# Optimization experiments

Measured on AMD Instinct MI355X. Metric: run time of the kernel, lower is better.

Reference implementation:

```python
import jax, jax.numpy as jnp
import numpy as np

T, B, V, F = 30, 32, 32, 128   # len_pred, batch, n_vehicles, feature_size
L, LF = 256, 64                # n_lanes, lane_feature_size
H = 8                          # n_heads
DH = F // H                    # head dim
HIST = 10                      # leading mask dim reduced by any()


def setup_inputs() -> dict:
    key = jax.random.key(0)
    ks = jax.random.split(key, 16)
    s = 0.05
    return {
        "vehicles":    jax.random.normal(ks[0], (T, B, V, F), jnp.float32),
        "initial_pos": jax.random.normal(ks[1], (T, B, V, F), jnp.float32),
        "lanes":       jax.random.normal(ks[2], (B, L, LF), jnp.float32),
        "mask_lanes":  jax.random.randint(ks[3], (HIST, B, L), 0, 2).astype(bool),
        # key_lanes / value_lanes: Linear(LF -> F)
        "Wk": jax.random.normal(ks[4], (F, LF), jnp.float32) * s,
        "bk": jax.random.normal(ks[5], (F,), jnp.float32) * s,
        "Wv": jax.random.normal(ks[6], (F, LF), jnp.float32) * s,
        "bv": jax.random.normal(ks[7], (F,), jnp.float32) * s,
        # query / relation_lanes: Conv2d(F, F, (1,1)) == pointwise Linear(F -> F)
        "Wq": jax.random.normal(ks[8], (F, F), jnp.float32) * s,
        "bq": jax.random.normal(ks[9], (F,), jnp.float32) * s,
        "Wr": jax.random.normal(ks[10], (F, F), jnp.float32) * s,
        "br": jax.random.normal(ks[11], (F,), jnp.float32) * s,
        # attention_combine: Linear(F -> F)
        "Wc": jax.random.normal(ks[12], (F, F), jnp.float32) * s,
        "bc": jax.random.normal(ks[13], (F,), jnp.float32) * s,
    }


def reference(vehicles, initial_pos, lanes, mask_lanes,
              Wk, bk, Wv, bv, Wq, bq, Wr, br, Wc, bc):
    v = vehicles + initial_pos                                   # [T,B,V,F]
    # lane projections -> [B,H,L,DH]
    k = (lanes @ Wk.T + bk).reshape(B, L, H, DH).transpose(0, 2, 1, 3)
    val = (lanes @ Wv.T + bv).reshape(B, L, H, DH).transpose(0, 2, 1, 3)
    # vehicle projections (1x1 conv == linear over feature dim) -> [T,B,H,V,DH]
    q = (v @ Wq.T + bq).reshape(T, B, V, H, DH).transpose(0, 1, 3, 2, 4)
    r = (v @ Wr.T + br).reshape(T, B, V, H, DH).transpose(0, 1, 3, 2, 4)
    # mask: any over leading dims -> [B,L]
    mask = jnp.any(mask_lanes, axis=0)
    scores = jnp.einsum('tbhvd,bhld->tbhvl', q, k) / jnp.sqrt(jnp.float32(DH))
    scores = jnp.where(mask[None, :, None, None, :], scores, jnp.float32(-1e9))
    p = jax.nn.softmax(scores, axis=-1)                          # [T,B,H,V,L]
    att = jnp.exp(jnp.einsum('tbhvl,bhld->tbhvd', p, jax.nn.log_sigmoid(val)))
    # faithful to original: raw reshape [T,B,H,V,DH] -> [T,B,V,F] (no permute back)
    out = (r * att).reshape(T, B, V, F)
    return out @ Wc.T + bc + v - 2.0 * initial_pos
```

## Files before the change

kernel.cpp:

```cpp
#include <hip/hip_runtime.h>
#include <hip/hip_bf16.h>
#include <math.h>

#define T_ 30
#define B_ 32
#define V_ 32
#define F_ 128
#define L_ 256
#define LF_ 64
#define H_ 8
#define DH_ 16
#define HIST_ 10

typedef __attribute__((ext_vector_type(4))) float floatx4;
typedef __attribute__((ext_vector_type(8))) short shortx8;
typedef __attribute__((ext_vector_type(4))) unsigned short ushortx4;

#define MFMA_BF16(a, b, c) __builtin_amdgcn_mfma_f32_16x16x32_bf16(a, b, c, 0, 0, 0)

__device__ inline unsigned short f2bf_rne(float x) {
    unsigned int u = __builtin_bit_cast(unsigned int, x);
    unsigned int r = (u + 0x7fffu + ((u >> 16) & 1u)) >> 16;
    return (unsigned short)r;
}
__device__ inline unsigned short f2bf_trunc(float x) {
    return (unsigned short)(__builtin_bit_cast(unsigned int, x) >> 16);
}
__device__ inline ushortx4 cvt4(floatx4 a) {
    ushortx4 r;
    r.x = f2bf_rne(a.x); r.y = f2bf_rne(a.y);
    r.z = f2bf_rne(a.z); r.w = f2bf_rne(a.w);
    return r;
}

__global__ void k_mask(const int* __restrict__ m, float* __restrict__ mb) {
    int idx = blockIdx.x * 256 + threadIdx.x;
    if (idx >= B_ * L_) return;
    int any = 0;
#pragma unroll
    for (int h = 0; h < HIST_; ++h) any |= m[h * (B_ * L_) + idx];
    mb[idx] = any ? 1.0f : 0.0f;
}

__global__ __launch_bounds__(256, 2) void k_lanes(
    const float* __restrict__ lanes, const float* __restrict__ Wk,
    const float* __restrict__ bk, const float* __restrict__ Wv,
    const float* __restrict__ bv, unsigned short* __restrict__ kproj,
    unsigned short* __restrict__ lsv) {
    __shared__ unsigned short WkF[8192];
    __shared__ unsigned short WvF[8192];
    int tid = threadIdx.x;
    for (int g = tid; g < 1024; g += 256) {
        int frag = g >> 6, l = g & 63, cc = l & 15, qq = l >> 4;
        int nt = frag >> 1, ks = frag & 1;
        int n = nt * 16 + cc, k0 = ks * 32 + qq * 8;
        floatx4 a0 = *(const floatx4*)(Wk + n * LF_ + k0);
        floatx4 a1 = *(const floatx4*)(Wk + n * LF_ + k0 + 4);
        *(ushortx4*)(WkF + g * 8) = cvt4(a0);
        *(ushortx4*)(WkF + g * 8 + 4) = cvt4(a1);
        floatx4 b0 = *(const floatx4*)(Wv + n * LF_ + k0);
        floatx4 b1 = *(const floatx4*)(Wv + n * LF_ + k0 + 4);
        *(ushortx4*)(WvF + g * 8) = cvt4(b0);
        *(ushortx4*)(WvF + g * 8 + 4) = cvt4(b1);
    }
    __syncthreads();
    int lane = tid & 63, w = tid >> 6;
    int c = lane & 15, quad = lane >> 4;
    int m0 = blockIdx.x * 64 + w * 16;
    shortx8 aF[2];
#pragma unroll
    for (int ks = 0; ks < 2; ++ks) {
        const float* xp = lanes + (size_t)(m0 + c) * LF_ + ks * 32 + quad * 8;
        floatx4 x0 = *(const floatx4*)(xp);
        floatx4 x1 = *(const floatx4*)(xp + 4);
        ushortx4 lo = cvt4(x0), hi = cvt4(x1);
        shortx8 af;
        af[0]=(short)lo.x; af[1]=(short)lo.y; af[2]=(short)lo.z; af[3]=(short)lo.w;
        af[4]=(short)hi.x; af[5]=(short)hi.y; af[6]=(short)hi.z; af[7]=(short)hi.w;
        aF[ks] = af;
    }
#pragma unroll
    for (int nt = 0; nt < 8; ++nt) {
        floatx4 acck = {0.f, 0.f, 0.f, 0.f}, accv = {0.f, 0.f, 0.f, 0.f};
#pragma unroll
        for (int ks = 0; ks < 2; ++ks) {
            shortx8 bkf = *(const shortx8*)(WkF + ((nt * 2 + ks) * 64 + lane) * 8);
            shortx8 bvf = *(const shortx8*)(WvF + ((nt * 2 + ks) * 64 + lane) * 8);
            acck = MFMA_BF16(aF[ks], bkf, acck);
            accv = MFMA_BF16(aF[ks], bvf, accv);
        }
        int n = nt * 16 + c;
        float bkn = bk[n], bvn = bv[n];
#pragma unroll
        for (int reg = 0; reg < 4; ++reg) {
            size_t row = m0 + quad * 4 + reg;
            kproj[row * F_ + n] = f2bf_rne(acck[reg] + bkn);
            float xv = accv[reg] + bvn;
            float ls = fminf(xv, 0.f) - log1pf(__expf(-fabsf(xv)));
            lsv[row * F_ + n] = f2bf_rne(ls);
        }
    }
}

__global__ __launch_bounds__(256, 2) void k_qr(
    const float* __restrict__ veh, const float* __restrict__ ip,
    const float* __restrict__ Wq, const float* __restrict__ bq,
    const float* __restrict__ Wr, const float* __restrict__ br,
    unsigned short* __restrict__ qb, float* __restrict__ rb) {
    __shared__ unsigned short WqF[16384];
    __shared__ unsigned short WrF[16384];
    int tid = threadIdx.x;
    for (int g = tid; g < 2048; g += 256) {
        int frag = g >> 6, l = g & 63, cc = l & 15, qq = l >> 4;
        int nt = frag >> 2, ks = frag & 3;
        int n = nt * 16 + cc, k0 = ks * 32 + qq * 8;
        floatx4 a0 = *(const floatx4*)(Wq + n * F_ + k0);
        floatx4 a1 = *(const floatx4*)(Wq + n * F_ + k0 + 4);
        *(ushortx4*)(WqF + g * 8) = cvt4(a0);
        *(ushortx4*)(WqF + g * 8 + 4) = cvt4(a1);
        floatx4 b0 = *(const floatx4*)(Wr + n * F_ + k0);
        floatx4 b1 = *(const floatx4*)(Wr + n * F_ + k0 + 4);
        *(ushortx4*)(WrF + g * 8) = cvt4(b0);
        *(ushortx4*)(WrF + g * 8 + 4) = cvt4(b1);
    }
    __syncthreads();
    int lane = tid & 63, w = tid >> 6;
    int c = lane & 15, quad = lane >> 4;
    int m0 = blockIdx.x * 64 + w * 16;
    shortx8 aF[4];
#pragma unroll
    for (int ks = 0; ks < 4; ++ks) {
        size_t off = (size_t)(m0 + c) * F_ + ks * 32 + quad * 8;
        floatx4 v0 = *(const floatx4*)(veh + off);
        floatx4 v1 = *(const floatx4*)(veh + off + 4);
        floatx4 i0 = *(const floatx4*)(ip + off);
        floatx4 i1 = *(const floatx4*)(ip + off + 4);
        ushortx4 lo = cvt4(v0 + i0), hi = cvt4(v1 + i1);
        shortx8 af;
        af[0]=(short)lo.x; af[1]=(short)lo.y; af[2]=(short)lo.z; af[3]=(short)lo.w;
        af[4]=(short)hi.x; af[5]=(short)hi.y; af[6]=(short)hi.z; af[7]=(short)hi.w;
        aF[ks] = af;
    }
#pragma unroll
    for (int nt = 0; nt < 8; ++nt) {
        floatx4 accq = {0.f, 0.f, 0.f, 0.f}, accr = {0.f, 0.f, 0.f, 0.f};
#pragma unroll
        for (int ks = 0; ks < 4; ++ks) {
            shortx8 bqf = *(const shortx8*)(WqF + ((nt * 4 + ks) * 64 + lane) * 8);
            shortx8 brf = *(const shortx8*)(WrF + ((nt * 4 + ks) * 64 + lane) * 8);
            accq = MFMA_BF16(aF[ks], bqf, accq);
            accr = MFMA_BF16(aF[ks], brf, accr);
        }
        int n = nt * 16 + c;
        float bqn = bq[n], brn = br[n];
#pragma unroll
        for (int reg = 0; reg < 4; ++reg) {
            size_t row = m0 + quad * 4 + reg;
            qb[row * F_ + n] = f2bf_rne((accq[reg] + bqn) * 0.25f);
            rb[row * F_ + n] = accr[reg] + brn;
        }
    }
}

__global__ __launch_bounds__(256, 2) void k_attn(
    const unsigned short* __restrict__ kproj, const unsigned short* __restrict__ lsv,
    const float* __restrict__ maskb, const unsigned short* __restrict__ qbuf,
    const float* __restrict__ rbuf, unsigned short* __restrict__ ratt) {
    __shared__ unsigned short kS[256 * 24];
    __shared__ unsigned short vT[16 * 264];
    __shared__ unsigned short pE[4 * 16 * 264];
    __shared__ float mS[256];

    int tid = threadIdx.x;
    int bh = blockIdx.x & 255;
    int tc = blockIdx.x >> 8;
    int h = bh & 7;
    int b = bh >> 3;

    const unsigned short* kbase = kproj + ((size_t)b * L_) * F_ + h * DH_;
    const unsigned short* vbase = lsv   + ((size_t)b * L_) * F_ + h * DH_;
#pragma unroll
    for (int it = 0; it < 2; ++it) {
        int id = it * 256 + tid;
        int l = id >> 1, half = id & 1;
        shortx8 kv = *(const shortx8*)(kbase + (size_t)l * F_ + half * 8);
        *(shortx8*)(kS + l * 24 + half * 8) = kv;
        shortx8 vv = *(const shortx8*)(vbase + (size_t)l * F_ + half * 8);
#pragma unroll
        for (int j = 0; j < 8; ++j)
            vT[(half * 8 + j) * 264 + l] = (unsigned short)vv[j];
    }
    mS[tid] = maskb[b * L_ + tid];
    __syncthreads();

    int lane = tid & 63, w = tid >> 6;
    int c = lane & 15, quad = lane >> 4;

    unsigned int mreg[4] = {0u, 0u, 0u, 0u};
#pragma unroll
    for (int lt = 0; lt < 16; ++lt) {
        floatx4 mv = *(const floatx4*)(mS + lt * 16 + quad * 4);
#pragma unroll
        for (int reg = 0; reg < 4; ++reg)
            mreg[reg] |= (mv[reg] > 0.5f ? 1u : 0u) << lt;
    }

    shortx8 kF[16];
#pragma unroll
    for (int lt = 0; lt < 16; ++lt) {
        shortx8 z = {0, 0, 0, 0, 0, 0, 0, 0};
        kF[lt] = (quad < 2) ? *(const shortx8*)(kS + (lt * 16 + c) * 24 + quad * 8) : z;
    }
    shortx8 vF[8];
#pragma unroll
    for (int kk = 0; kk < 8; ++kk)
        vF[kk] = *(const shortx8*)(vT + c * 264 + kk * 32 + quad * 8);

    unsigned short* pEw = pE + w * (16 * 264);

    for (int i = 0; i < 4; ++i) {
        int mtl = i * 4 + w;
        bool act = mtl < 15;
        int mt = tc * 15 + mtl;
        int q0 = mt << 4;
        int t = q0 >> 5, v0 = q0 & 31;
        size_t qrow0 = ((size_t)(t * B_ + b) * V_ + v0 + c) * F_ + h * DH_;
        float sum = 0.f;
        floatx4 cS[16];

        if (act) {
            shortx8 qF = {0, 0, 0, 0, 0, 0, 0, 0};
            if (quad < 2) qF = *(const shortx8*)(qbuf + qrow0 + quad * 8);
            floatx4 z4 = {0.f, 0.f, 0.f, 0.f};
#pragma unroll
            for (int lt = 0; lt < 16; ++lt)
                cS[lt] = MFMA_BF16(kF[lt], qF, z4);

            float mx = -3.0e38f;
#pragma unroll
            for (int lt = 0; lt < 16; ++lt)
                mx = fmaxf(mx, fmaxf(fmaxf(cS[lt][0], cS[lt][1]),
                                     fmaxf(cS[lt][2], cS[lt][3])));
            mx = fmaxf(mx, __shfl_xor(mx, 16));
            mx = fmaxf(mx, __shfl_xor(mx, 32));

#pragma unroll
            for (int lt = 0; lt < 16; ++lt) {
                ushortx4 ep;
#pragma unroll
                for (int reg = 0; reg < 4; ++reg) {
                    float bitf = (float)((mreg[reg] >> lt) & 1u);
                    float e = __expf(cS[lt][reg] - mx) * bitf;
                    sum += e;
                    ep[reg] = f2bf_trunc(e);
                }
                *(ushortx4*)(pEw + c * 264 + lt * 16 + quad * 4) = ep;
            }
            sum += __shfl_xor(sum, 16);
            sum += __shfl_xor(sum, 32);
        }
        __syncthreads();

        if (act) {
            floatx4 cU = {0.f, 0.f, 0.f, 0.f};
#pragma unroll
            for (int kk = 0; kk < 8; ++kk) {
                shortx8 bP = *(const shortx8*)(pEw + c * 264 + kk * 32 + quad * 8);
                cU = MFMA_BF16(vF[kk], bP, cU);
            }
            float inv = __builtin_amdgcn_rcpf(sum);
            floatx4 rv = *(const floatx4*)(rbuf + qrow0 + quad * 4);
            ushortx4 ob;
#pragma unroll
            for (int reg = 0; reg < 4; ++reg)
                ob[reg] = f2bf_rne(rv[reg] * __expf(cU[reg] * inv));
            *(ushortx4*)(ratt + (((size_t)t * B_ + b) * H_ + h) * (V_ * DH_)
                        + (v0 + c) * DH_ + quad * 4) = ob;
        }
        __syncthreads();
    }
}

__global__ __launch_bounds__(256, 2) void k_out(
    const unsigned short* __restrict__ ratt, const float* __restrict__ Wc,
    const float* __restrict__ bc, const float* __restrict__ veh,
    const float* __restrict__ ip, float* __restrict__ out) {
    __shared__ unsigned short WcF[16384];
    int tid = threadIdx.x;
    for (int g = tid; g < 2048; g += 256) {
        int frag = g >> 6, l = g & 63, cc = l & 15, qq = l >> 4;
        int nt = frag >> 2, ks = frag & 3;
        int n = nt * 16 + cc, k0 = ks * 32 + qq * 8;
        floatx4 a0 = *(const floatx4*)(Wc + n * F_ + k0);
        floatx4 a1 = *(const floatx4*)(Wc + n * F_ + k0 + 4);
        *(ushortx4*)(WcF + g * 8) = cvt4(a0);
        *(ushortx4*)(WcF + g * 8 + 4) = cvt4(a1);
    }
    __syncthreads();
    int lane = tid & 63, w = tid >> 6;
    int c = lane & 15, quad = lane >> 4;
    int m0 = blockIdx.x * 64 + w * 16;
    shortx8 aF[4];
#pragma unroll
    for (int ks = 0; ks < 4; ++ks)
        aF[ks] = *(const shortx8*)(ratt + (size_t)(m0 + c) * F_ + ks * 32 + quad * 8);
#pragma unroll
    for (int np = 0; np < 4; ++np) {
        int nt0 = np * 2, nt1 = np * 2 + 1;
        floatx4 acc0 = {0.f, 0.f, 0.f, 0.f}, acc1 = {0.f, 0.f, 0.f, 0.f};
#pragma unroll
        for (int ks = 0; ks < 4; ++ks) {
            shortx8 b0 = *(const shortx8*)(WcF + ((nt0 * 4 + ks) * 64 + lane) * 8);
            shortx8 b1 = *(const shortx8*)(WcF + ((nt1 * 4 + ks) * 64 + lane) * 8);
            acc0 = MFMA_BF16(aF[ks], b0, acc0);
            acc1 = MFMA_BF16(aF[ks], b1, acc1);
        }
        int n0 = nt0 * 16 + c, n1 = nt1 * 16 + c;
        float bc0 = bc[n0], bc1 = bc[n1];
#pragma unroll
        for (int reg = 0; reg < 4; ++reg) {
            size_t row = m0 + quad * 4 + reg;
            size_t o0 = row * F_ + n0, o1 = row * F_ + n1;
            out[o0] = acc0[reg] + bc0 + veh[o0] - ip[o0];
            out[o1] = acc1[reg] + bc1 + veh[o1] - ip[o1];
        }
    }
}

extern "C" void kernel_launch(void* const* d_in, const int* in_sizes, int n_in,
                              void* d_out, int out_size, void* d_ws, size_t ws_size,
                              hipStream_t stream) {
    const float* vehicles    = (const float*)d_in[0];
    const float* initial_pos = (const float*)d_in[1];
    const float* lanes       = (const float*)d_in[2];
    const int*   mask        = (const int*)d_in[3];
    const float* Wk = (const float*)d_in[4];
    const float* bk = (const float*)d_in[5];
    const float* Wv = (const float*)d_in[6];
    const float* bv = (const float*)d_in[7];
    const float* Wq = (const float*)d_in[8];
    const float* bq = (const float*)d_in[9];
    const float* Wr = (const float*)d_in[10];
    const float* br = (const float*)d_in[11];
    const float* Wc = (const float*)d_in[12];
    const float* bc = (const float*)d_in[13];
    float* out = (float*)d_out;

    char* p = (char*)d_ws;
    float* maskb = (float*)p;          p += ((B_ * L_ * 4 + 255) / 256) * 256;
    unsigned short* kproj = (unsigned short*)p; p += ((size_t)B_ * L_ * F_ * 2 + 255) / 256 * 256;
    unsigned short* lsvb  = (unsigned short*)p; p += ((size_t)B_ * L_ * F_ * 2 + 255) / 256 * 256;
    unsigned short* qb    = (unsigned short*)p; p += ((size_t)T_ * B_ * V_ * F_ * 2 + 255) / 256 * 256;
    float* rb             = (float*)p;          p += ((size_t)T_ * B_ * V_ * F_ * 4 + 255) / 256 * 256;
    unsigned short* rattb = (unsigned short*)p; p += ((size_t)T_ * B_ * V_ * F_ * 2 + 255) / 256 * 256;

    k_mask<<<(B_ * L_ + 255) / 256, 256, 0, stream>>>(mask, maskb);
    k_lanes<<<(B_ * L_) / 64, 256, 0, stream>>>(lanes, Wk, bk, Wv, bv, kproj, lsvb);
    k_qr<<<(T_ * B_ * V_) / 64, 256, 0, stream>>>(vehicles, initial_pos, Wq, bq, Wr, br, qb, rb);
    k_attn<<<4 * B_ * H_, 256, 0, stream>>>(kproj, lsvb, maskb, qb, rb, rattb);
    k_out<<<(T_ * B_ * V_) / 64, 256, 0, stream>>>(rattb, Wc, bc, vehicles, initial_pos, out);
}
```

Baseline: 178.0 us.

## Fuse mask into lane kernel, drop softmax max pass, use MFMA for normalizer

Several changes at once. The mask reduction moves into the lane projection kernel, removing one launch. The log-sigmoid values are stored pre-masked and transposed so the attention kernel loads them with vector copies. The r projection is stored in bf16 to halve its traffic. The softmax skips the max subtraction, works in base 2 with exp2, and gets its masked denominator from an extra MFMA against a mask fragment, which removes the per-tile syncthreads. Dropping the max subtraction risks overflow when scores are large.

```diff
diff --git a/kernel.cpp b/kernel.cpp
--- a/kernel.cpp
+++ b/kernel.cpp
@@ -26,6 +26,9 @@
 __device__ inline unsigned short f2bf_trunc(float x) {
     return (unsigned short)(__builtin_bit_cast(unsigned int, x) >> 16);
 }
+__device__ inline float bf2f(unsigned short u) {
+    return __builtin_bit_cast(float, (unsigned int)u << 16);
+}
 __device__ inline ushortx4 cvt4(floatx4 a) {
     ushortx4 r;
     r.x = f2bf_rne(a.x); r.y = f2bf_rne(a.y);
@@ -33,23 +36,27 @@
     return r;
 }
 
-__global__ void k_mask(const int* __restrict__ m, float* __restrict__ mb) {
-    int idx = blockIdx.x * 256 + threadIdx.x;
-    if (idx >= B_ * L_) return;
-    int any = 0;
-#pragma unroll
-    for (int h = 0; h < HIST_; ++h) any |= m[h * (B_ * L_) + idx];
-    mb[idx] = any ? 1.0f : 0.0f;
-}
-
 __global__ __launch_bounds__(256, 2) void k_lanes(
-    const float* __restrict__ lanes, const float* __restrict__ Wk,
-    const float* __restrict__ bk, const float* __restrict__ Wv,
-    const float* __restrict__ bv, unsigned short* __restrict__ kproj,
-    unsigned short* __restrict__ lsv) {
+    const float* __restrict__ lanes, const int* __restrict__ mask,
+    const float* __restrict__ Wk, const float* __restrict__ bk,
+    const float* __restrict__ Wv, const float* __restrict__ bv,
+    unsigned short* __restrict__ kproj, unsigned short* __restrict__ lsvT,
+    float* __restrict__ maskb) {
     __shared__ unsigned short WkF[8192];
     __shared__ unsigned short WvF[8192];
+    __shared__ float mloc[64];
     int tid = threadIdx.x;
+    int m0 = blockIdx.x * 64;
+    int b = m0 >> 8;
+    if (tid < 64) {
+        int row = m0 + tid;
+        int any = 0;
+#pragma unroll
+        for (int hh = 0; hh < HIST_; ++hh) any |= mask[hh * (B_ * L_) + row];
+        float fm = any ? 1.0f : 0.0f;
+        maskb[row] = fm;
+        mloc[tid] = fm;
+    }
     for (int g = tid; g < 1024; g += 256) {
         int frag = g >> 6, l = g & 63, cc = l & 15, qq = l >> 4;
         int nt = frag >> 1, ks = frag & 1;
@@ -66,11 +73,11 @@
     __syncthreads();
     int lane = tid & 63, w = tid >> 6;
     int c = lane & 15, quad = lane >> 4;
-    int m0 = blockIdx.x * 64 + w * 16;
+    int mw = m0 + w * 16;
     shortx8 aF[2];
 #pragma unroll
     for (int ks = 0; ks < 2; ++ks) {
-        const float* xp = lanes + (size_t)(m0 + c) * LF_ + ks * 32 + quad * 8;
+        const float* xp = lanes + (size_t)(mw + c) * LF_ + ks * 32 + quad * 8;
         floatx4 x0 = *(const floatx4*)(xp);
         floatx4 x1 = *(const floatx4*)(xp + 4);
         ushortx4 lo = cvt4(x0), hi = cvt4(x1);
@@ -79,6 +86,8 @@
         af[4]=(short)hi.x; af[5]=(short)hi.y; af[6]=(short)hi.z; af[7]=(short)hi.w;
         aF[ks] = af;
     }
+    floatx4 mk = *(const floatx4*)(mloc + w * 16 + quad * 4);
+    int lbase = (mw & 255) + quad * 4;
 #pragma unroll
     for (int nt = 0; nt < 8; ++nt) {
         floatx4 acck = {0.f, 0.f, 0.f, 0.f}, accv = {0.f, 0.f, 0.f, 0.f};
@@ -91,14 +100,16 @@
         }
         int n = nt * 16 + c;
         float bkn = bk[n], bvn = bv[n];
+        ushortx4 vout;
 #pragma unroll
         for (int reg = 0; reg < 4; ++reg) {
-            size_t row = m0 + quad * 4 + reg;
+            size_t row = mw + quad * 4 + reg;
             kproj[row * F_ + n] = f2bf_rne(acck[reg] + bkn);
             float xv = accv[reg] + bvn;
             float ls = fminf(xv, 0.f) - log1pf(__expf(-fabsf(xv)));
-            lsv[row * F_ + n] = f2bf_rne(ls);
-        }
+            vout[reg] = (mk[reg] > 0.5f) ? f2bf_rne(ls) : (unsigned short)0;
+        }
+        *(ushortx4*)(lsvT + ((size_t)b * F_ + n) * L_ + lbase) = vout;
     }
 }
 
@@ -106,7 +117,7 @@
     const float* __restrict__ veh, const float* __restrict__ ip,
     const float* __restrict__ Wq, const float* __restrict__ bq,
     const float* __restrict__ Wr, const float* __restrict__ br,
-    unsigned short* __restrict__ qb, float* __restrict__ rb) {
+    unsigned short* __restrict__ qb, unsigned short* __restrict__ rb) {
     __shared__ unsigned short WqF[16384];
     __shared__ unsigned short WrF[16384];
     int tid = threadIdx.x;
@@ -141,6 +152,7 @@
         af[4]=(short)hi.x; af[5]=(short)hi.y; af[6]=(short)hi.z; af[7]=(short)hi.w;
         aF[ks] = af;
     }
+    const float QSCALE = 0.25f * 1.4426950408889634f;
 #pragma unroll
     for (int nt = 0; nt < 8; ++nt) {
         floatx4 accq = {0.f, 0.f, 0.f, 0.f}, accr = {0.f, 0.f, 0.f, 0.f};
@@ -156,20 +168,19 @@
 #pragma unroll
         for (int reg = 0; reg < 4; ++reg) {
             size_t row = m0 + quad * 4 + reg;
-            qb[row * F_ + n] = f2bf_rne((accq[reg] + bqn) * 0.25f);
-            rb[row * F_ + n] = accr[reg] + brn;
+            qb[row * F_ + n] = f2bf_rne((accq[reg] + bqn) * QSCALE);
+            rb[row * F_ + n] = f2bf_rne(accr[reg] + brn);
         }
     }
 }
 
 __global__ __launch_bounds__(256, 2) void k_attn(
-    const unsigned short* __restrict__ kproj, const unsigned short* __restrict__ lsv,
+    const unsigned short* __restrict__ kproj, const unsigned short* __restrict__ lsvT,
     const float* __restrict__ maskb, const unsigned short* __restrict__ qbuf,
-    const float* __restrict__ rbuf, unsigned short* __restrict__ ratt) {
+    const unsigned short* __restrict__ rbuf, unsigned short* __restrict__ ratt) {
     __shared__ unsigned short kS[256 * 24];
     __shared__ unsigned short vT[16 * 264];
     __shared__ unsigned short pE[4 * 16 * 264];
-    __shared__ float mS[256];
 
     int tid = threadIdx.x;
     int bh = blockIdx.x & 255;
@@ -178,32 +189,25 @@
     int b = bh >> 3;
 
     const unsigned short* kbase = kproj + ((size_t)b * L_) * F_ + h * DH_;
-    const unsigned short* vbase = lsv   + ((size_t)b * L_) * F_ + h * DH_;
 #pragma unroll
     for (int it = 0; it < 2; ++it) {
         int id = it * 256 + tid;
         int l = id >> 1, half = id & 1;
         shortx8 kv = *(const shortx8*)(kbase + (size_t)l * F_ + half * 8);
         *(shortx8*)(kS + l * 24 + half * 8) = kv;
-        shortx8 vv = *(const shortx8*)(vbase + (size_t)l * F_ + half * 8);
-#pragma unroll
-        for (int j = 0; j < 8; ++j)
-            vT[(half * 8 + j) * 264 + l] = (unsigned short)vv[j];
-    }
-    mS[tid] = maskb[b * L_ + tid];
+    }
+    {
+        int d = tid >> 4, c16 = tid & 15;
+        const unsigned short* vrow = lsvT + ((size_t)b * F_ + h * DH_ + d) * L_ + c16 * 16;
+        shortx8 v0 = *(const shortx8*)(vrow);
+        shortx8 v1 = *(const shortx8*)(vrow + 8);
+        *(shortx8*)(vT + d * 264 + c16 * 16) = v0;
+        *(shortx8*)(vT + d * 264 + c16 * 16 + 8) = v1;
+    }
     __syncthreads();
 
     int lane = tid & 63, w = tid >> 6;
     int c = lane & 15, quad = lane >> 4;
-
-    unsigned int mreg[4] = {0u, 0u, 0u, 0u};
-#pragma unroll
-    for (int lt = 0; lt < 16; ++lt) {
-        floatx4 mv = *(const floatx4*)(mS + lt * 16 + quad * 4);
-#pragma unroll
-        for (int reg = 0; reg < 4; ++reg)
-            mreg[reg] |= (mv[reg] > 0.5f ? 1u : 0u) << lt;
-    }
 
     shortx8 kF[16];
 #pragma unroll
@@ -215,69 +219,59 @@
 #pragma unroll
     for (int kk = 0; kk < 8; ++kk)
         vF[kk] = *(const shortx8*)(vT + c * 264 + kk * 32 + quad * 8);
+    shortx8 mF[8];
+#pragma unroll
+    for (int kk = 0; kk < 8; ++kk) {
+        const float* mp = maskb + b * L_ + kk * 32 + quad * 8;
+        floatx4 ma = *(const floatx4*)(mp);
+        floatx4 mb2 = *(const floatx4*)(mp + 4);
+        shortx8 mf;
+        mf[0]=(short)f2bf_trunc(ma.x); mf[1]=(short)f2bf_trunc(ma.y);
+        mf[2]=(short)f2bf_trunc(ma.z); mf[3]=(short)f2bf_trunc(ma.w);
+        mf[4]=(short)f2bf_trunc(mb2.x); mf[5]=(short)f2bf_trunc(mb2.y);
+        mf[6]=(short)f2bf_trunc(mb2.z); mf[7]=(short)f2bf_trunc(mb2.w);
+        mF[kk] = mf;
+    }
 
     unsigned short* pEw = pE + w * (16 * 264);
-
-    for (int i = 0; i < 4; ++i) {
-        int mtl = i * 4 + w;
-        bool act = mtl < 15;
+    floatx4 z4 = {0.f, 0.f, 0.f, 0.f};
+
+    for (int mtl = w; mtl < 15; mtl += 4) {
         int mt = tc * 15 + mtl;
         int q0 = mt << 4;
         int t = q0 >> 5, v0 = q0 & 31;
         size_t qrow0 = ((size_t)(t * B_ + b) * V_ + v0 + c) * F_ + h * DH_;
-        float sum = 0.f;
-        floatx4 cS[16];
-
-        if (act) {
-            shortx8 qF = {0, 0, 0, 0, 0, 0, 0, 0};
-            if (quad < 2) qF = *(const shortx8*)(qbuf + qrow0 + quad * 8);
-            floatx4 z4 = {0.f, 0.f, 0.f, 0.f};
-#pragma unroll
-            for (int lt = 0; lt < 16; ++lt)
-                cS[lt] = MFMA_BF16(kF[lt], qF, z4);
-
-            float mx = -3.0e38f;
-#pragma unroll
-            for (int lt = 0; lt < 16; ++lt)
-                mx = fmaxf(mx, fmaxf(fmaxf(cS[lt][0], cS[lt][1]),
-                                     fmaxf(cS[lt][2], cS[lt][3])));
-            mx = fmaxf(mx, __shfl_xor(mx, 16));
-            mx = fmaxf(mx, __shfl_xor(mx, 32));
-
-#pragma unroll
-            for (int lt = 0; lt < 16; ++lt) {
-                ushortx4 ep;
-#pragma unroll
-                for (int reg = 0; reg < 4; ++reg) {
-                    float bitf = (float)((mreg[reg] >> lt) & 1u);
-                    float e = __expf(cS[lt][reg] - mx) * bitf;
-                    sum += e;
-                    ep[reg] = f2bf_trunc(e);
-                }
-                *(ushortx4*)(pEw + c * 264 + lt * 16 + quad * 4) = ep;
-            }
-            sum += __shfl_xor(sum, 16);
-            sum += __shfl_xor(sum, 32);
-        }
-        __syncthreads();
-
-        if (act) {
-            floatx4 cU = {0.f, 0.f, 0.f, 0.f};
-#pragma unroll
-            for (int kk = 0; kk < 8; ++kk) {
-                shortx8 bP = *(const shortx8*)(pEw + c * 264 + kk * 32 + quad * 8);
-                cU = MFMA_BF16(vF[kk], bP, cU);
-            }
-            float inv = __builtin_amdgcn_rcpf(sum);
-            floatx4 rv = *(const floatx4*)(rbuf + qrow0 + quad * 4);
-            ushortx4 ob;
+
+        shortx8 qF = {0, 0, 0, 0, 0, 0, 0, 0};
+        if (quad < 2) qF = *(const shortx8*)(qbuf + qrow0 + quad * 8);
+
+#pragma unroll
+        for (int lt = 0; lt < 16; ++lt) {
+            floatx4 s = MFMA_BF16(kF[lt], qF, z4);
+            ushortx4 ep;
 #pragma unroll
             for (int reg = 0; reg < 4; ++reg)
-                ob[reg] = f2bf_rne(rv[reg] * __expf(cU[reg] * inv));
-            *(ushortx4*)(ratt + (((size_t)t * B_ + b) * H_ + h) * (V_ * DH_)
-                        + (v0 + c) * DH_ + quad * 4) = ob;
-        }
-        __syncthreads();
+                ep[reg] = f2bf_trunc(__builtin_amdgcn_exp2f(s[reg]));
+            *(ushortx4*)(pEw + c * 264 + lt * 16 + quad * 4) = ep;
+        }
+
+        floatx4 cU = z4, cN = z4;
+#pragma unroll
+        for (int kk = 0; kk < 8; ++kk) {
+            shortx8 bP = *(const shortx8*)(pEw + c * 264 + kk * 32 + quad * 8);
+            cU = MFMA_BF16(vF[kk], bP, cU);
+            cN = MFMA_BF16(mF[kk], bP, cN);
+        }
+        float inv2 = __builtin_amdgcn_rcpf(cN[0]) * 1.4426950408889634f;
+        ushortx4 rv = *(const ushortx4*)(rbuf + qrow0 + quad * 4);
+        ushortx4 ob;
+#pragma unroll
+        for (int reg = 0; reg < 4; ++reg) {
+            float att = __builtin_amdgcn_exp2f(cU[reg] * inv2);
+            ob[reg] = f2bf_rne(bf2f(rv[reg]) * att);
+        }
+        *(ushortx4*)(ratt + (((size_t)t * B_ + b) * H_ + h) * (V_ * DH_)
+                    + (v0 + c) * DH_ + quad * 4) = ob;
     }
 }
 
@@ -347,16 +341,15 @@
     float* out = (float*)d_out;
 
     char* p = (char*)d_ws;
-    float* maskb = (float*)p;          p += ((B_ * L_ * 4 + 255) / 256) * 256;
+    float* maskb = (float*)p;                   p += ((B_ * L_ * 4 + 255) / 256) * 256;
     unsigned short* kproj = (unsigned short*)p; p += ((size_t)B_ * L_ * F_ * 2 + 255) / 256 * 256;
-    unsigned short* lsvb  = (unsigned short*)p; p += ((size_t)B_ * L_ * F_ * 2 + 255) / 256 * 256;
+    unsigned short* lsvT  = (unsigned short*)p; p += ((size_t)B_ * F_ * L_ * 2 + 255) / 256 * 256;
     unsigned short* qb    = (unsigned short*)p; p += ((size_t)T_ * B_ * V_ * F_ * 2 + 255) / 256 * 256;
-    float* rb             = (float*)p;          p += ((size_t)T_ * B_ * V_ * F_ * 4 + 255) / 256 * 256;
+    unsigned short* rb    = (unsigned short*)p; p += ((size_t)T_ * B_ * V_ * F_ * 2 + 255) / 256 * 256;
     unsigned short* rattb = (unsigned short*)p; p += ((size_t)T_ * B_ * V_ * F_ * 2 + 255) / 256 * 256;
 
-    k_mask<<<(B_ * L_ + 255) / 256, 256, 0, stream>>>(mask, maskb);
-    k_lanes<<<(B_ * L_) / 64, 256, 0, stream>>>(lanes, Wk, bk, Wv, bv, kproj, lsvb);
+    k_lanes<<<(B_ * L_) / 64, 256, 0, stream>>>(lanes, mask, Wk, bk, Wv, bv, kproj, lsvT, maskb);
     k_qr<<<(T_ * B_ * V_) / 64, 256, 0, stream>>>(vehicles, initial_pos, Wq, bq, Wr, br, qb, rb);
-    k_attn<<<4 * B_ * H_, 256, 0, stream>>>(kproj, lsvb, maskb, qb, rb, rattb);
+    k_attn<<<4 * B_ * H_, 256, 0, stream>>>(kproj, lsvT, maskb, qb, rb, rattb);
     k_out<<<(T_ * B_ * V_) / 64, 256, 0, stream>>>(rattb, Wc, bc, vehicles, initial_pos, out);
 }
```

Result: faster. 168.3 us (-5.4%).
